# Kernel tuning notes

Measured on AMD Instinct MI355X. Metric: run time of the kernel, lower is better.

Reference implementation:

```python
import jax, jax.numpy as jnp
import numpy as np


def setup_inputs() -> dict:
    key = jax.random.key(0)
    ks = jax.random.split(key, 12)
    N, D, E = 50000, 64, 320000
    H0, H1, H2, OUT = 4 * D, 128, 128, 1  # edgemlp_size=[256,128,128], out_features=1
    h1 = jax.random.normal(ks[0], (N, D), dtype=jnp.float32)
    h2 = jax.random.normal(ks[1], (N, D), dtype=jnp.float32)
    src = jax.random.randint(ks[2], (E,), 0, N, dtype=jnp.int64)
    dst = jax.random.randint(ks[3], (E,), 0, N, dtype=jnp.int64)
    def lin_init(kw, kb, fan_in, fan_out):
        bound = 1.0 / np.sqrt(fan_in)
        W = jax.random.uniform(kw, (fan_out, fan_in), minval=-bound, maxval=bound, dtype=jnp.float32)
        b = jax.random.uniform(kb, (fan_out,), minval=-bound, maxval=bound, dtype=jnp.float32)
        return W, b
    W1, b1 = lin_init(ks[4], ks[5], H0, H1)
    W2, b2 = lin_init(ks[6], ks[7], H1, H2)
    W3, b3 = lin_init(ks[8], ks[9], H2, OUT)
    return {"h1": h1, "h2": h2, "src": src, "dst": dst,
            "W1": W1, "b1": b1, "W2": W2, "b2": b2, "W3": W3, "b3": b3}


def reference(h1, h2, src, dst, W1, b1, W2, b2, W3, b3):
    # Gather per-edge node features. NOTE: original code uses edges.src['h2']
    # for BOTH h2_u and h2_v (faithful to source), so h2 is gathered by src twice.
    h1_u = h1[src]            # [E, D]
    h1_v = h1[dst]            # [E, D]
    h2_u = h2[src]            # [E, D]
    h2_v = h2[src]            # [E, D]  (src, per original)
    h = jnp.concatenate([h1_u, h1_v, h2_u, h2_v], axis=1)  # [E, 4D]
    h = jax.nn.sigmoid(h @ W1.T + b1)
    h = jax.nn.sigmoid(h @ W2.T + b2)
    score = h @ W3.T + b3     # [E, out_features]
    return score
```

## Files before the change

### kernel.cpp

```cpp
#include <hip/hip_runtime.h>
#include <hip/hip_bf16.h>
#include <cstdint>


typedef __attribute__((ext_vector_type(8))) short bf16x8;
typedef __attribute__((ext_vector_type(4))) float f32x4;

__device__ __forceinline__ float sigmoid_fast(float x) {
    float e = __expf(-x);
    return __builtin_amdgcn_rcpf(1.0f + e);
}
__device__ __forceinline__ ushort f2bf_rne(float f) {
    uint32_t u = __float_as_uint(f);
    return (ushort)((u + 0x7fffu + ((u >> 16) & 1u)) >> 16);
}
__device__ __forceinline__ float bf2f_lo(uint32_t d) { return __uint_as_float(d << 16); }
__device__ __forceinline__ float bf2f_hi(uint32_t d) { return __uint_as_float(d & 0xffff0000u); }
__device__ __forceinline__ uint32_t packbf_rhu(float x, float y) {
    return ((__float_as_uint(x) + 0x8000u) >> 16) |
           ((__float_as_uint(y) + 0x8000u) & 0xffff0000u);
}

__global__ void prep_kernel(const float* __restrict__ W1, const float* __restrict__ W2,
                            ushort* __restrict__ WCF, ushort* __restrict__ WBF,
                            ushort* __restrict__ W2F) {
    int i = blockIdx.x * blockDim.x + threadIdx.x;
    if (i >= 16384) return;
    int j = i & 7, lf = (i >> 3) & 63, nt = (i >> 9) & 7, kk = i >> 12;
    int n = nt * 16 + (lf & 15);
    int kpos = kk * 32 + ((lf >> 4) << 3) + j;
    int ktrue = (kpos & ~31) | ((kpos >> 1) & 15) | ((kpos & 1) << 4);
    W2F[i] = f2bf_rne(W2[n * 128 + ktrue]);
    float v = (kpos < 64) ? W1[n * 256 + kpos]
                          : W1[n * 256 + 128 + (kpos - 64)] + W1[n * 256 + 192 + (kpos - 64)];
    WCF[i] = f2bf_rne(v);
    if (kk < 2) WBF[i] = f2bf_rne(W1[n * 256 + 64 + kpos]);
}

__global__ __launch_bounds__(256, 4) void node_kernel(
    const float* __restrict__ h1, const float* __restrict__ h2,
    const ushort* __restrict__ WCF, const ushort* __restrict__ WBF,
    const float* __restrict__ b1,
    uint32_t* __restrict__ Aout, uint32_t* __restrict__ Bout, int N)
{
    __shared__ __align__(16) ushort xt[64 * 136];
    const int tid = threadIdx.x, g = tid >> 6, ln = tid & 63;
    const int nl = ln & 15, q = ln >> 4;
    const int n0 = blockIdx.x * 64;
    const bool full = (n0 + 64 <= N);

    bf16x8 fa[4][2], fb[2][2];
    #pragma unroll
    for (int kk = 0; kk < 4; ++kk)
        #pragma unroll
        for (int nt = 0; nt < 2; ++nt)
            fa[kk][nt] = *(const bf16x8*)(WCF + (((kk * 8 + g * 2 + nt) * 64 + ln) << 3));
    #pragma unroll
    for (int kk = 0; kk < 2; ++kk)
        #pragma unroll
        for (int nt = 0; nt < 2; ++nt)
            fb[kk][nt] = *(const bf16x8*)(WBF + (((kk * 8 + g * 2 + nt) * 64 + ln) << 3));
    const float b1c0 = b1[g * 32 + nl], b1c1 = b1[g * 32 + 16 + nl];

    #pragma unroll
    for (int i = 0; i < 8; ++i) {
        int local = i * 256 + tid;
        int node = local >> 5;
        int kq = (local & 31) * 4;
        float4 x = make_float4(0.f, 0.f, 0.f, 0.f);
        if (full || n0 + node < N)
            x = (kq < 64) ? *(const float4*)(h1 + (size_t)(n0 + node) * 64 + kq)
                          : *(const float4*)(h2 + (size_t)(n0 + node) * 64 + (kq - 64));
        uint32_t d0 = packbf_rhu(x.x, x.y), d1 = packbf_rhu(x.z, x.w);
        *(uint2*)&xt[node * 136 + kq] = make_uint2(d0, d1);
    }
    __syncthreads();

    #pragma unroll
    for (int m = 0; m < 4; ++m) {
        f32x4 accA[2], accB[2];
        #pragma unroll
        for (int r = 0; r < 4; ++r) { accA[0][r] = accA[1][r] = accB[0][r] = accB[1][r] = 0.f; }
        const ushort* arow = &xt[(m * 16 + nl) * 136 + (q << 3)];
        #pragma unroll
        for (int kk = 0; kk < 4; ++kk) {
            bf16x8 a = *(const bf16x8*)(arow + kk * 32);
            accA[0] = __builtin_amdgcn_mfma_f32_16x16x32_bf16(a, fa[kk][0], accA[0], 0, 0, 0);
            accA[1] = __builtin_amdgcn_mfma_f32_16x16x32_bf16(a, fa[kk][1], accA[1], 0, 0, 0);
            if (kk < 2) {
                accB[0] = __builtin_amdgcn_mfma_f32_16x16x32_bf16(a, fb[kk][0], accB[0], 0, 0, 0);
                accB[1] = __builtin_amdgcn_mfma_f32_16x16x32_bf16(a, fb[kk][1], accB[1], 0, 0, 0);
            }
        }
        #pragma unroll
        for (int r = 0; r < 4; ++r) {
            int node = n0 + m * 16 + q * 4 + r;
            if (full || node < N) {
                Aout[(size_t)node * 64 + g * 16 + nl] = packbf_rhu(accA[0][r] + b1c0, accA[1][r] + b1c1);
                Bout[(size_t)node * 64 + g * 16 + nl] = packbf_rhu(accB[0][r], accB[1][r]);
            }
        }
    }
}

__global__ __launch_bounds__(64, 2) void edge_kernel(
    const uint32_t* __restrict__ Am, const uint32_t* __restrict__ Bm,
    const int* __restrict__ src, const int* __restrict__ dst,
    const ushort* __restrict__ W2F, const float* __restrict__ b2,
    const float* __restrict__ W3, const float* __restrict__ b3,
    float* __restrict__ out, int E, int ngroups)
{
    __shared__ __align__(16) ushort hlds[16 * 136];
    const int ln = threadIdx.x;
    const int nl = ln & 15, q = ln >> 4;
    const int el = ln >> 2, p = ln & 3;

    bf16x8 bfrag[32];
    #pragma unroll
    for (int kk = 0; kk < 4; ++kk)
        #pragma unroll
        for (int nt = 0; nt < 8; ++nt)
            bfrag[kk * 8 + nt] =
                *(const bf16x8*)(W2F + (((kk * 8 + nt) * 64 + ln) << 3));
    float b2c[8], w3c[8];
    #pragma unroll
    for (int nt = 0; nt < 8; ++nt) {
        b2c[nt] = b2[nt * 16 + nl];
        w3c[nt] = W3[nt * 16 + nl];
    }
    const float b3c = b3[0];

    uint4 ga[4], gb[4];
    int grp = blockIdx.x;
    if (grp < ngroups) {
        int eb = grp * 16, us = 0, vs = 0;
        if (ln < 16 && eb + ln < E) { us = src[eb + ln]; vs = dst[eb + ln]; }
        int uu = __shfl(us, el), vv = __shfl(vs, el);
        const uint32_t* ap = Am + (size_t)uu * 64 + p * 4;
        const uint32_t* bp = Bm + (size_t)vv * 64 + p * 4;
        #pragma unroll
        for (int r = 0; r < 4; ++r) {
            ga[r] = *(const uint4*)(ap + r * 16);
            gb[r] = *(const uint4*)(bp + r * 16);
        }
    }
    for (; grp < ngroups; grp += gridDim.x) {
        const int tn = grp + (int)gridDim.x;
        int us = 0, vs = 0;
        if (tn < ngroups) {
            int eb2 = tn * 16;
            if (ln < 16 && eb2 + ln < E) { us = src[eb2 + ln]; vs = dst[eb2 + ln]; }
        }

        #pragma unroll
        for (int r = 0; r < 4; ++r) {
            uint32_t sa[4] = {ga[r].x, ga[r].y, ga[r].z, ga[r].w};
            uint32_t sb[4] = {gb[r].x, gb[r].y, gb[r].z, gb[r].w};
            uint32_t da[4];
            #pragma unroll
            for (int d = 0; d < 4; ++d) {
                float zl = bf2f_lo(sa[d]) + bf2f_lo(sb[d]);
                float zh = bf2f_hi(sa[d]) + bf2f_hi(sb[d]);
                da[d] = packbf_rhu(sigmoid_fast(zl), sigmoid_fast(zh));
            }
            *(uint4*)&hlds[el * 136 + r * 32 + p * 8] =
                make_uint4(da[0], da[1], da[2], da[3]);
        }
        if (tn < ngroups) {
            int uu = __shfl(us, el), vv = __shfl(vs, el);
            const uint32_t* ap = Am + (size_t)uu * 64 + p * 4;
            const uint32_t* bp = Bm + (size_t)vv * 64 + p * 4;
            #pragma unroll
            for (int r = 0; r < 4; ++r) {
                ga[r] = *(const uint4*)(ap + r * 16);
                gb[r] = *(const uint4*)(bp + r * 16);
            }
        }

        const ushort* arow = &hlds[nl * 136 + (q << 3)];
        bf16x8 a0 = *(const bf16x8*)(arow);
        bf16x8 a1 = *(const bf16x8*)(arow + 32);
        bf16x8 a2 = *(const bf16x8*)(arow + 64);
        bf16x8 a3 = *(const bf16x8*)(arow + 96);

        float pr[4] = {0.f, 0.f, 0.f, 0.f};
        #pragma unroll
        for (int np = 0; np < 4; ++np) {
            const int n0t = 2 * np, n1t = 2 * np + 1;
            f32x4 acc0 = {0.f, 0.f, 0.f, 0.f}, acc1 = {0.f, 0.f, 0.f, 0.f};
            acc0 = __builtin_amdgcn_mfma_f32_16x16x32_bf16(a0, bfrag[n0t],      acc0, 0, 0, 0);
            acc1 = __builtin_amdgcn_mfma_f32_16x16x32_bf16(a0, bfrag[n1t],      acc1, 0, 0, 0);
            acc0 = __builtin_amdgcn_mfma_f32_16x16x32_bf16(a1, bfrag[8 + n0t],  acc0, 0, 0, 0);
            acc1 = __builtin_amdgcn_mfma_f32_16x16x32_bf16(a1, bfrag[8 + n1t],  acc1, 0, 0, 0);
            acc0 = __builtin_amdgcn_mfma_f32_16x16x32_bf16(a2, bfrag[16 + n0t], acc0, 0, 0, 0);
            acc1 = __builtin_amdgcn_mfma_f32_16x16x32_bf16(a2, bfrag[16 + n1t], acc1, 0, 0, 0);
            acc0 = __builtin_amdgcn_mfma_f32_16x16x32_bf16(a3, bfrag[24 + n0t], acc0, 0, 0, 0);
            acc1 = __builtin_amdgcn_mfma_f32_16x16x32_bf16(a3, bfrag[24 + n1t], acc1, 0, 0, 0);
            #pragma unroll
            for (int r = 0; r < 4; ++r) {
                pr[r] = fmaf(w3c[n0t], sigmoid_fast(acc0[r] + b2c[n0t]), pr[r]);
                pr[r] = fmaf(w3c[n1t], sigmoid_fast(acc1[r] + b2c[n1t]), pr[r]);
            }
        }
        #pragma unroll
        for (int r = 0; r < 4; ++r) {
            pr[r] += __shfl_xor(pr[r], 1, 16);
            pr[r] += __shfl_xor(pr[r], 2, 16);
            pr[r] += __shfl_xor(pr[r], 4, 16);
            pr[r] += __shfl_xor(pr[r], 8, 16);
        }
        if (nl == 0) {
            int eo = grp * 16 + q * 4;
            if (eo + 4 <= E) {
                *(float4*)(out + eo) = make_float4(pr[0] + b3c, pr[1] + b3c,
                                                   pr[2] + b3c, pr[3] + b3c);
            } else {
                #pragma unroll
                for (int r = 0; r < 4; ++r)
                    if (eo + r < E) out[eo + r] = pr[r] + b3c;
            }
        }
    }
}

__global__ void naive_kernel(
    const float* __restrict__ h1, const float* __restrict__ h2,
    const int* __restrict__ src, const int* __restrict__ dst,
    const float* __restrict__ W1, const float* __restrict__ b1,
    const float* __restrict__ W2, const float* __restrict__ b2,
    const float* __restrict__ W3, const float* __restrict__ b3,
    float* __restrict__ out, int E, int N)
{
    int e = blockIdx.x * blockDim.x + threadIdx.x;
    if (e >= E) return;
    int u = src[e], v = dst[e];
    float h[128];
    for (int j = 0; j < 128; ++j) {
        float z = b1[j];
        const float* wj = W1 + j * 256;
        for (int k = 0; k < 64; ++k) {
            z += wj[k] * h1[(size_t)u * 64 + k]
               + wj[64 + k] * h1[(size_t)v * 64 + k]
               + (wj[128 + k] + wj[192 + k]) * h2[(size_t)u * 64 + k];
        }
        h[j] = 1.0f / (1.0f + __expf(-z));
    }
    float gg[128];
    for (int j = 0; j < 128; ++j) {
        float z = b2[j];
        for (int k = 0; k < 128; ++k) z = fmaf(W2[j * 128 + k], h[k], z);
        gg[j] = 1.0f / (1.0f + __expf(-z));
    }
    float s = b3[0];
    for (int j = 0; j < 128; ++j) s = fmaf(W3[j], gg[j], s);
    out[e] = s;
}

extern "C" void kernel_launch(void* const* d_in, const int* in_sizes, int n_in,
                              void* d_out, int out_size, void* d_ws, size_t ws_size,
                              hipStream_t stream) {
    const float* h1 = (const float*)d_in[0];
    const float* h2 = (const float*)d_in[1];
    const int*  src = (const int*)d_in[2];
    const int*  dst = (const int*)d_in[3];
    const float* W1 = (const float*)d_in[4];
    const float* b1 = (const float*)d_in[5];
    const float* W2 = (const float*)d_in[6];
    const float* b2 = (const float*)d_in[7];
    const float* W3 = (const float*)d_in[8];
    const float* b3 = (const float*)d_in[9];
    float* out = (float*)d_out;

    const int N = in_sizes[0] / 64;
    const int E = in_sizes[2];

    size_t offA   = 0;
    size_t offB   = offA + (size_t)N * 64;
    size_t offWCF = offB + (size_t)N * 64;
    size_t offWBF = offWCF + 8192;
    size_t offW2F = offWBF + 4096;
    size_t totalF = offW2F + 8192;

    if (ws_size < totalF * sizeof(float)) {
        naive_kernel<<<(E + 255) / 256, 256, 0, stream>>>(
            h1, h2, src, dst, W1, b1, W2, b2, W3, b3, out, E, N);
        return;
    }

    float* ws = (float*)d_ws;
    ushort* WCF = (ushort*)(ws + offWCF);
    ushort* WBF = (ushort*)(ws + offWBF);
    ushort* W2F = (ushort*)(ws + offW2F);

    prep_kernel<<<64, 256, 0, stream>>>(W1, W2, WCF, WBF, W2F);
    node_kernel<<<(N + 63) / 64, 256, 0, stream>>>(
        h1, h2, WCF, WBF, b1, (uint32_t*)(ws + offA), (uint32_t*)(ws + offB), N);
    const int ngroups = (E + 15) / 16;
    edge_kernel<<<2000, 64, 0, stream>>>(
        (const uint32_t*)(ws + offA), (const uint32_t*)(ws + offB), src, dst,
        W2F, b2, W3, b3, out, E, ngroups);
}
```

Baseline: 132.2 us.

## Load MFMA A-fragments directly from global and fold -log2e into weights

Both kernels drop their LDS staging. The node kernel builds bf16 MFMA A-fragments directly from h1/h2 rows, and the edge kernel gathers Am/Bm per lane in the MFMA fragment layout, then applies the sigmoid in registers. The -log2(e) factor is folded into W1, W2, b1 and b2 during prep, so the sigmoid becomes exp2 plus rcp with no multiply. This removes shared-memory round trips and barriers, at the cost of less coalesced global reads. The node kernel's launch bound is also lowered from 4 to 3 blocks per SM.

```diff
diff --git a/kernel.cpp b/kernel.cpp
--- a/kernel.cpp
+++ b/kernel.cpp
@@ -6,8 +6,10 @@
 typedef __attribute__((ext_vector_type(8))) short bf16x8;
 typedef __attribute__((ext_vector_type(4))) float f32x4;
 
-__device__ __forceinline__ float sigmoid_fast(float x) {
-    float e = __expf(-x);
+#define NEG_LOG2E (-1.44269504f)
+
+__device__ __forceinline__ float sig_from_t(float t) {
+    float e = __builtin_amdgcn_exp2f(t);
     return __builtin_amdgcn_rcpf(1.0f + e);
 }
 __device__ __forceinline__ ushort f2bf_rne(float f) {
@@ -19,6 +21,18 @@
 __device__ __forceinline__ uint32_t packbf_rhu(float x, float y) {
     return ((__float_as_uint(x) + 0x8000u) >> 16) |
            ((__float_as_uint(y) + 0x8000u) & 0xffff0000u);
+}
+union frag_cvt { uint4 u; bf16x8 h; };
+__device__ __forceinline__ bf16x8 pack8(float4 a, float4 b) {
+    frag_cvt c;
+    c.u = make_uint4(packbf_rhu(a.x, a.y), packbf_rhu(a.z, a.w),
+                     packbf_rhu(b.x, b.y), packbf_rhu(b.z, b.w));
+    return c.h;
+}
+__device__ __forceinline__ uint32_t sig2_pack(uint32_t ua, uint32_t ub) {
+    float tl = bf2f_lo(ua) + bf2f_lo(ub);
+    float th = bf2f_hi(ua) + bf2f_hi(ub);
+    return packbf_rhu(sig_from_t(tl), sig_from_t(th));
 }
 
 __global__ void prep_kernel(const float* __restrict__ W1, const float* __restrict__ W2,
@@ -30,24 +44,22 @@
     int n = nt * 16 + (lf & 15);
     int kpos = kk * 32 + ((lf >> 4) << 3) + j;
     int ktrue = (kpos & ~31) | ((kpos >> 1) & 15) | ((kpos & 1) << 4);
-    W2F[i] = f2bf_rne(W2[n * 128 + ktrue]);
+    W2F[i] = f2bf_rne(NEG_LOG2E * W2[n * 128 + ktrue]);
     float v = (kpos < 64) ? W1[n * 256 + kpos]
                           : W1[n * 256 + 128 + (kpos - 64)] + W1[n * 256 + 192 + (kpos - 64)];
-    WCF[i] = f2bf_rne(v);
-    if (kk < 2) WBF[i] = f2bf_rne(W1[n * 256 + 64 + kpos]);
-}
-
-__global__ __launch_bounds__(256, 4) void node_kernel(
+    WCF[i] = f2bf_rne(NEG_LOG2E * v);
+    if (kk < 2) WBF[i] = f2bf_rne(NEG_LOG2E * W1[n * 256 + 64 + kpos]);
+}
+
+__global__ __launch_bounds__(256, 3) void node_kernel(
     const float* __restrict__ h1, const float* __restrict__ h2,
     const ushort* __restrict__ WCF, const ushort* __restrict__ WBF,
     const float* __restrict__ b1,
     uint32_t* __restrict__ Aout, uint32_t* __restrict__ Bout, int N)
 {
-    __shared__ __align__(16) ushort xt[64 * 136];
     const int tid = threadIdx.x, g = tid >> 6, ln = tid & 63;
     const int nl = ln & 15, q = ln >> 4;
     const int n0 = blockIdx.x * 64;
-    const bool full = (n0 + 64 <= N);
 
     bf16x8 fa[4][2], fb[2][2];
     #pragma unroll
@@ -60,42 +72,47 @@
         #pragma unroll
         for (int nt = 0; nt < 2; ++nt)
             fb[kk][nt] = *(const bf16x8*)(WBF + (((kk * 8 + g * 2 + nt) * 64 + ln) << 3));
-    const float b1c0 = b1[g * 32 + nl], b1c1 = b1[g * 32 + 16 + nl];
-
-    #pragma unroll
-    for (int i = 0; i < 8; ++i) {
-        int local = i * 256 + tid;
-        int node = local >> 5;
-        int kq = (local & 31) * 4;
-        float4 x = make_float4(0.f, 0.f, 0.f, 0.f);
-        if (full || n0 + node < N)
-            x = (kq < 64) ? *(const float4*)(h1 + (size_t)(n0 + node) * 64 + kq)
-                          : *(const float4*)(h2 + (size_t)(n0 + node) * 64 + (kq - 64));
-        uint32_t d0 = packbf_rhu(x.x, x.y), d1 = packbf_rhu(x.z, x.w);
-        *(uint2*)&xt[node * 136 + kq] = make_uint2(d0, d1);
-    }
-    __syncthreads();
+    const float b1c0 = NEG_LOG2E * b1[g * 32 + nl];
+    const float b1c1 = NEG_LOG2E * b1[g * 32 + 16 + nl];
 
     #pragma unroll
     for (int m = 0; m < 4; ++m) {
+        const int row = n0 + m * 16 + nl;
+        const bool ok = row < N;
+        const float* r1 = h1 + (size_t)row * 64 + q * 8;
+        const float* r2 = h2 + (size_t)row * 64 + q * 8;
+        const float4 z4 = make_float4(0.f, 0.f, 0.f, 0.f);
+        float4 xa, xb;
+        bf16x8 af[4];
+        xa = ok ? *(const float4*)(r1)      : z4;
+        xb = ok ? *(const float4*)(r1 + 4)  : z4;
+        af[0] = pack8(xa, xb);
+        xa = ok ? *(const float4*)(r1 + 32) : z4;
+        xb = ok ? *(const float4*)(r1 + 36) : z4;
+        af[1] = pack8(xa, xb);
+        xa = ok ? *(const float4*)(r2)      : z4;
+        xb = ok ? *(const float4*)(r2 + 4)  : z4;
+        af[2] = pack8(xa, xb);
+        xa = ok ? *(const float4*)(r2 + 32) : z4;
+        xb = ok ? *(const float4*)(r2 + 36) : z4;
+        af[3] = pack8(xa, xb);
+
         f32x4 accA[2], accB[2];
         #pragma unroll
         for (int r = 0; r < 4; ++r) { accA[0][r] = accA[1][r] = accB[0][r] = accB[1][r] = 0.f; }
-        const ushort* arow = &xt[(m * 16 + nl) * 136 + (q << 3)];
         #pragma unroll
         for (int kk = 0; kk < 4; ++kk) {
-            bf16x8 a = *(const bf16x8*)(arow + kk * 32);
-            accA[0] = __builtin_amdgcn_mfma_f32_16x16x32_bf16(a, fa[kk][0], accA[0], 0, 0, 0);
-            accA[1] = __builtin_amdgcn_mfma_f32_16x16x32_bf16(a, fa[kk][1], accA[1], 0, 0, 0);
+            accA[0] = __builtin_amdgcn_mfma_f32_16x16x32_bf16(af[kk], fa[kk][0], accA[0], 0, 0, 0);
+            accA[1] = __builtin_amdgcn_mfma_f32_16x16x32_bf16(af[kk], fa[kk][1], accA[1], 0, 0, 0);
             if (kk < 2) {
-                accB[0] = __builtin_amdgcn_mfma_f32_16x16x32_bf16(a, fb[kk][0], accB[0], 0, 0, 0);
-                accB[1] = __builtin_amdgcn_mfma_f32_16x16x32_bf16(a, fb[kk][1], accB[1], 0, 0, 0);
+                accB[0] = __builtin_amdgcn_mfma_f32_16x16x32_bf16(af[kk], fb[kk][0], accB[0], 0, 0, 0);
+                accB[1] = __builtin_amdgcn_mfma_f32_16x16x32_bf16(af[kk], fb[kk][1], accB[1], 0, 0, 0);
             }
         }
         #pragma unroll
         for (int r = 0; r < 4; ++r) {
             int node = n0 + m * 16 + q * 4 + r;
-            if (full || node < N) {
+            if (node < N) {
                 Aout[(size_t)node * 64 + g * 16 + nl] = packbf_rhu(accA[0][r] + b1c0, accA[1][r] + b1c1);
                 Bout[(size_t)node * 64 + g * 16 + nl] = packbf_rhu(accB[0][r], accB[1][r]);
             }
@@ -110,10 +127,8 @@
     const float* __restrict__ W3, const float* __restrict__ b3,
     float* __restrict__ out, int E, int ngroups)
 {
-    __shared__ __align__(16) ushort hlds[16 * 136];
     const int ln = threadIdx.x;
     const int nl = ln & 15, q = ln >> 4;
-    const int el = ln >> 2, p = ln & 3;
 
     bf16x8 bfrag[32];
     #pragma unroll
@@ -125,7 +140,7 @@
     float b2c[8], w3c[8];
     #pragma unroll
     for (int nt = 0; nt < 8; ++nt) {
-        b2c[nt] = b2[nt * 16 + nl];
+        b2c[nt] = NEG_LOG2E * b2[nt * 16 + nl];
         w3c[nt] = W3[nt * 16 + nl];
     }
     const float b3c = b3[0];
@@ -135,13 +150,13 @@
     if (grp < ngroups) {
         int eb = grp * 16, us = 0, vs = 0;
         if (ln < 16 && eb + ln < E) { us = src[eb + ln]; vs = dst[eb + ln]; }
-        int uu = __shfl(us, el), vv = __shfl(vs, el);
-        const uint32_t* ap = Am + (size_t)uu * 64 + p * 4;
-        const uint32_t* bp = Bm + (size_t)vv * 64 + p * 4;
-        #pragma unroll
-        for (int r = 0; r < 4; ++r) {
-            ga[r] = *(const uint4*)(ap + r * 16);
-            gb[r] = *(const uint4*)(bp + r * 16);
+        int uu = __shfl(us, nl), vv = __shfl(vs, nl);
+        const uint32_t* ap = Am + (size_t)uu * 64 + q * 4;
+        const uint32_t* bp = Bm + (size_t)vv * 64 + q * 4;
+        #pragma unroll
+        for (int kk = 0; kk < 4; ++kk) {
+            ga[kk] = *(const uint4*)(ap + kk * 16);
+            gb[kk] = *(const uint4*)(bp + kk * 16);
         }
     }
     for (; grp < ngroups; grp += gridDim.x) {
@@ -152,54 +167,41 @@
             if (ln < 16 && eb2 + ln < E) { us = src[eb2 + ln]; vs = dst[eb2 + ln]; }
         }
 
-        #pragma unroll
-        for (int r = 0; r < 4; ++r) {
-            uint32_t sa[4] = {ga[r].x, ga[r].y, ga[r].z, ga[r].w};
-            uint32_t sb[4] = {gb[r].x, gb[r].y, gb[r].z, gb[r].w};
-            uint32_t da[4];
+        bf16x8 af[4];
+        #pragma unroll
+        for (int kk = 0; kk < 4; ++kk) {
+            frag_cvt c;
+            c.u = make_uint4(sig2_pack(ga[kk].x, gb[kk].x),
+                             sig2_pack(ga[kk].y, gb[kk].y),
+                             sig2_pack(ga[kk].z, gb[kk].z),
+                             sig2_pack(ga[kk].w, gb[kk].w));
+            af[kk] = c.h;
+        }
+        if (tn < ngroups) {
+            int uu = __shfl(us, nl), vv = __shfl(vs, nl);
+            const uint32_t* ap = Am + (size_t)uu * 64 + q * 4;
+            const uint32_t* bp = Bm + (size_t)vv * 64 + q * 4;
             #pragma unroll
-            for (int d = 0; d < 4; ++d) {
-                float zl = bf2f_lo(sa[d]) + bf2f_lo(sb[d]);
-                float zh = bf2f_hi(sa[d]) + bf2f_hi(sb[d]);
-                da[d] = packbf_rhu(sigmoid_fast(zl), sigmoid_fast(zh));
-            }
-            *(uint4*)&hlds[el * 136 + r * 32 + p * 8] =
-                make_uint4(da[0], da[1], da[2], da[3]);
-        }
-        if (tn < ngroups) {
-            int uu = __shfl(us, el), vv = __shfl(vs, el);
-            const uint32_t* ap = Am + (size_t)uu * 64 + p * 4;
-            const uint32_t* bp = Bm + (size_t)vv * 64 + p * 4;
-            #pragma unroll
-            for (int r = 0; r < 4; ++r) {
-                ga[r] = *(const uint4*)(ap + r * 16);
-                gb[r] = *(const uint4*)(bp + r * 16);
-            }
-        }
-
-        const ushort* arow = &hlds[nl * 136 + (q << 3)];
-        bf16x8 a0 = *(const bf16x8*)(arow);
-        bf16x8 a1 = *(const bf16x8*)(arow + 32);
-        bf16x8 a2 = *(const bf16x8*)(arow + 64);
-        bf16x8 a3 = *(const bf16x8*)(arow + 96);
+            for (int kk = 0; kk < 4; ++kk) {
+                ga[kk] = *(const uint4*)(ap + kk * 16);
+                gb[kk] = *(const uint4*)(bp + kk * 16);
+            }
+        }
 
         float pr[4] = {0.f, 0.f, 0.f, 0.f};
         #pragma unroll
         for (int np = 0; np < 4; ++np) {
             const int n0t = 2 * np, n1t = 2 * np + 1;
             f32x4 acc0 = {0.f, 0.f, 0.f, 0.f}, acc1 = {0.f, 0.f, 0.f, 0.f};
-            acc0 = __builtin_amdgcn_mfma_f32_16x16x32_bf16(a0, bfrag[n0t],      acc0, 0, 0, 0);
-            acc1 = __builtin_amdgcn_mfma_f32_16x16x32_bf16(a0, bfrag[n1t],      acc1, 0, 0, 0);
-            acc0 = __builtin_amdgcn_mfma_f32_16x16x32_bf16(a1, bfrag[8 + n0t],  acc0, 0, 0, 0);
-            acc1 = __builtin_amdgcn_mfma_f32_16x16x32_bf16(a1, bfrag[8 + n1t],  acc1, 0, 0, 0);
-            acc0 = __builtin_amdgcn_mfma_f32_16x16x32_bf16(a2, bfrag[16 + n0t], acc0, 0, 0, 0);
-            acc1 = __builtin_amdgcn_mfma_f32_16x16x32_bf16(a2, bfrag[16 + n1t], acc1, 0, 0, 0);
-            acc0 = __builtin_amdgcn_mfma_f32_16x16x32_bf16(a3, bfrag[24 + n0t], acc0, 0, 0, 0);
-            acc1 = __builtin_amdgcn_mfma_f32_16x16x32_bf16(a3, bfrag[24 + n1t], acc1, 0, 0, 0);
+            #pragma unroll
+            for (int kk = 0; kk < 4; ++kk) {
+                acc0 = __builtin_amdgcn_mfma_f32_16x16x32_bf16(af[kk], bfrag[kk * 8 + n0t], acc0, 0, 0, 0);
+                acc1 = __builtin_amdgcn_mfma_f32_16x16x32_bf16(af[kk], bfrag[kk * 8 + n1t], acc1, 0, 0, 0);
+            }
             #pragma unroll
             for (int r = 0; r < 4; ++r) {
-                pr[r] = fmaf(w3c[n0t], sigmoid_fast(acc0[r] + b2c[n0t]), pr[r]);
-                pr[r] = fmaf(w3c[n1t], sigmoid_fast(acc1[r] + b2c[n1t]), pr[r]);
+                pr[r] = fmaf(w3c[n0t], sig_from_t(acc0[r] + b2c[n0t]), pr[r]);
+                pr[r] = fmaf(w3c[n1t], sig_from_t(acc1[r] + b2c[n1t]), pr[r]);
             }
         }
         #pragma unroll
```

After: 187.7 us. 1.42x slower.
